# Kernel optimization log

Measured on AMD Instinct MI355X. Metric: run time of the kernel, lower is better.

Reference implementation:

```python
import jax, jax.numpy as jnp
import numpy as np

B, H, Wd, D, NC = 8, 64, 128, 272, 19   # batch, H/16, W/16, capsule feat dim, num_classes
P, NI = 524288, 4096                    # total points, total instances


def setup_inputs() -> dict:
    key = jax.random.key(0)
    k0, k1, k2, k3 = jax.random.split(key, 4)
    return {
        "class_capsules": jax.random.normal(k0, (B, H, Wd, D), dtype=jnp.float32),
        "W": jax.random.normal(k1, (D, NC), dtype=jnp.float32) * 0.05,
        "b": jnp.zeros((NC,), dtype=jnp.float32),
        "point_idx": jax.random.randint(k2, (P,), 0, B * H * Wd, dtype=jnp.int32),
        "segment_ids": jnp.sort(jax.random.randint(k3, (P,), 0, NI, dtype=jnp.int32)),
        "num_segments": NI,
    }


def reference(class_capsules, W, b, point_idx, segment_ids, num_segments):
    # Batched version of: inst_capsules = class_capsules[i, ys, xs, :];
    # pooled = mean(inst_capsules, 0); out = sigmoid(linear(pooled))
    # point_idx are flat (already deduped) indices into the [B*H*Wd] grid.
    feats = class_capsules.reshape(-1, class_capsules.shape[-1])[point_idx]        # [P, D]
    sums = jax.ops.segment_sum(feats, segment_ids, num_segments=num_segments)       # [NI, D]
    counts = jax.ops.segment_sum(jnp.ones((feats.shape[0],), feats.dtype),
                                 segment_ids, num_segments=num_segments)            # [NI]
    pooled = sums / jnp.maximum(counts, 1.0)[:, None]                                # mean pool
    return jax.nn.sigmoid(pooled @ W + b)                                            # [NI, NC]
```

## Files before the change

kernel.cpp:

```cpp
#include <hip/hip_runtime.h>
#include <math.h>

#define NROWS 65536
#define DD    272
#define NC    19
#define NP    524288
#define NSEG  4096
#define PS    20

#define PROJ_BLOCKS   (NROWS / 64)
#define BOUND_BLOCKS  (NP / 256)

__global__ __launch_bounds__(256) void proj_bounds_kernel(
    const float* __restrict__ X, const float* __restrict__ W,
    const int* __restrict__ seg, float* __restrict__ proj,
    int* __restrict__ bnd) {
  const int t = threadIdx.x;

  if (blockIdx.x >= PROJ_BLOCKS) {
    const int p = (blockIdx.x - PROJ_BLOCKS) * 256 + t;
    const int cur  = seg[p];
    const int prev = (p == 0) ? -1 : seg[p - 1];
    for (int s = prev + 1; s <= cur; ++s) bnd[s] = p;
    if (p == NP - 1) {
      for (int s = cur + 1; s <= NSEG; ++s) bnd[s] = NP;
    }
    return;
  }

  const int lane = t & 63;
  const int q    = __builtin_amdgcn_readfirstlane(t >> 6);
  const int row0 = blockIdx.x * 64;

  __shared__ float Xs[64 * 17];
  __shared__ float R[4 * 64 * NC];

  float acc[NC];
#pragma unroll
  for (int c = 0; c < NC; ++c) acc[c] = 0.f;

  const int r_ld = t >> 2;
  const int c4   = t & 3;
  const float* gsrc = X + (size_t)(row0 + r_ld) * DD + c4 * 4;

  float4 v = *(const float4*)gsrc;

  for (int chunk = 0; chunk < 17; ++chunk) {
    __syncthreads();
    float* dst = &Xs[r_ld * 17 + c4 * 4];
    dst[0] = v.x; dst[1] = v.y; dst[2] = v.z; dst[3] = v.w;
    __syncthreads();
    if (chunk < 16)
      v = *(const float4*)(gsrc + (chunk + 1) * 16);
    const int d0 = chunk * 16;
#pragma unroll
    for (int k = 0; k < 4; ++k) {
      const int c16 = q + 4 * k;
      const float x = Xs[lane * 17 + c16];
      const float* wr = W + (d0 + c16) * NC;
#pragma unroll
      for (int c = 0; c < NC; ++c) acc[c] = fmaf(x, wr[c], acc[c]);
    }
  }

#pragma unroll
  for (int c = 0; c < NC; ++c) R[(q * 64 + lane) * NC + c] = acc[c];
  __syncthreads();
#pragma unroll
  for (int j = 0; j < 5; ++j) {
    int f = t + 256 * j;
    int r = f / PS;
    int c = f % PS;
    float s = 0.f;
    if (c < NC) {
      s = R[r * NC + c] + R[(64 + r) * NC + c] +
          R[(128 + r) * NC + c] + R[(192 + r) * NC + c];
    }
    proj[(size_t)row0 * PS + f] = s;
  }
}

__global__ __launch_bounds__(64) void pool_kernel(
    const float* __restrict__ proj, const int* __restrict__ point_idx,
    const int* __restrict__ bnd, const float* __restrict__ bias,
    float* __restrict__ out) {
  const int s    = blockIdx.x;
  const int lane = threadIdx.x;
  const int start = bnd[s];
  const int end   = bnd[s + 1];

  float a[PS];
#pragma unroll
  for (int j = 0; j < PS; ++j) a[j] = 0.f;

  for (int p = start + lane; p < end; p += 64) {
    const int pi = point_idx[p];
    const float4* row = (const float4*)(proj + (size_t)pi * PS);
#pragma unroll
    for (int j = 0; j < 5; ++j) {
      float4 v = row[j];
      a[4 * j + 0] += v.x; a[4 * j + 1] += v.y;
      a[4 * j + 2] += v.z; a[4 * j + 3] += v.w;
    }
  }

#pragma unroll
  for (int off = 32; off > 0; off >>= 1) {
#pragma unroll
    for (int j = 0; j < NC; ++j) a[j] += __shfl_xor(a[j], off);
  }

  if (lane == 0) {
    const float inv = 1.f / fmaxf((float)(end - start), 1.f);
#pragma unroll
    for (int c = 0; c < NC; ++c) {
      float m = a[c] * inv + bias[c];
      out[s * NC + c] = 1.f / (1.f + expf(-m));
    }
  }
}

__global__ __launch_bounds__(256) void fallback_kernel(
    const float* __restrict__ X, const float* __restrict__ W,
    const float* __restrict__ bias, const int* __restrict__ point_idx,
    const int* __restrict__ seg, float* __restrict__ out) {
  const int s = blockIdx.x;
  const int t = threadIdx.x;
  __shared__ float Ps[DD];

  int lo = 0, hi = NP;
  while (lo < hi) { int mid = (lo + hi) >> 1; if (seg[mid] <  s) lo = mid + 1; else hi = mid; }
  const int start = lo;
  hi = NP;
  while (lo < hi) { int mid = (lo + hi) >> 1; if (seg[mid] <= s) lo = mid + 1; else hi = mid; }
  const int end = lo;

  float a0 = 0.f, a1 = 0.f;
  for (int p = start; p < end; ++p) {
    const int pi = point_idx[p];
    const float* row = X + (size_t)pi * DD;
    a0 += row[t];
    if (t < DD - 256) a1 += row[256 + t];
  }
  const float inv = 1.f / fmaxf((float)(end - start), 1.f);
  Ps[t] = a0 * inv;
  if (t < DD - 256) Ps[256 + t] = a1 * inv;
  __syncthreads();

  if (t < NC) {
    float acc = bias[t];
    for (int d = 0; d < DD; ++d) acc = fmaf(Ps[d], W[d * NC + t], acc);
    out[s * NC + t] = 1.f / (1.f + expf(-acc));
  }
}

extern "C" void kernel_launch(void* const* d_in, const int* in_sizes, int n_in,
                              void* d_out, int out_size, void* d_ws, size_t ws_size,
                              hipStream_t stream) {
  const float* X         = (const float*)d_in[0];
  const float* W         = (const float*)d_in[1];
  const float* bias      = (const float*)d_in[2];
  const int*   point_idx = (const int*)d_in[3];
  const int*   seg       = (const int*)d_in[4];
  float*       out       = (float*)d_out;

  const size_t proj_bytes = (size_t)NROWS * PS * sizeof(float);
  const size_t need = proj_bytes + (size_t)(NSEG + 1) * sizeof(int);
  if (ws_size >= need) {
    float* proj = (float*)d_ws;
    int*   bnd  = (int*)((char*)d_ws + proj_bytes);
    proj_bounds_kernel<<<PROJ_BLOCKS + BOUND_BLOCKS, 256, 0, stream>>>(
        X, W, seg, proj, bnd);
    pool_kernel<<<NSEG, 64, 0, stream>>>(proj, point_idx, bnd, bias, out);
  } else {
    fallback_kernel<<<NSEG, 256, 0, stream>>>(X, W, bias, point_idx, seg, out);
  }
}
```

Before: 128.7 us.

## Double-buffer projection tile loads and pack four segments per pool block

The projection kernel now double-buffers the shared-memory X tile and keeps two chunks of global loads in flight, which removes one barrier per chunk and hides load latency behind the FMAs. The pool kernel runs four segments per 256-thread block, one per wavefront, instead of one 64-thread block per segment. It also prefetches the next point index before the gathered row is accumulated. The trade-off is more shared memory and registers in the projection kernel.

```diff
diff --git a/kernel.cpp b/kernel.cpp
--- a/kernel.cpp
+++ b/kernel.cpp
@@ -32,7 +32,7 @@
   const int q    = __builtin_amdgcn_readfirstlane(t >> 6);
   const int row0 = blockIdx.x * 64;
 
-  __shared__ float Xs[64 * 17];
+  __shared__ float Xs[2][64 * 17];
   __shared__ float R[4 * 64 * NC];
 
   float acc[NC];
@@ -42,24 +42,37 @@
   const int r_ld = t >> 2;
   const int c4   = t & 3;
   const float* gsrc = X + (size_t)(row0 + r_ld) * DD + c4 * 4;
+  const int ldoff = r_ld * 17 + c4 * 4;
 
-  float4 v = *(const float4*)gsrc;
+  {
+    float4 v0 = *(const float4*)gsrc;
+    float* dst = &Xs[0][ldoff];
+    dst[0] = v0.x; dst[1] = v0.y; dst[2] = v0.z; dst[3] = v0.w;
+  }
+  float4 vv0 = *(const float4*)(gsrc + 16);
+  float4 vv1 = *(const float4*)(gsrc + 32);
+  __syncthreads();
 
   for (int chunk = 0; chunk < 17; ++chunk) {
-    __syncthreads();
-    float* dst = &Xs[r_ld * 17 + c4 * 4];
-    dst[0] = v.x; dst[1] = v.y; dst[2] = v.z; dst[3] = v.w;
-    __syncthreads();
-    if (chunk < 16)
-      v = *(const float4*)(gsrc + (chunk + 1) * 16);
     const int d0 = chunk * 16;
+    const float* xb = &Xs[chunk & 1][lane * 17];
 #pragma unroll
     for (int k = 0; k < 4; ++k) {
       const int c16 = q + 4 * k;
-      const float x = Xs[lane * 17 + c16];
+      const float x = xb[c16];
       const float* wr = W + (d0 + c16) * NC;
 #pragma unroll
       for (int c = 0; c < NC; ++c) acc[c] = fmaf(x, wr[c], acc[c]);
+    }
+    if (chunk < 16) {
+      float4 v = (chunk & 1) ? vv1 : vv0;
+      float* dst = &Xs[(chunk + 1) & 1][ldoff];
+      dst[0] = v.x; dst[1] = v.y; dst[2] = v.z; dst[3] = v.w;
+      __syncthreads();
+      if (chunk + 3 <= 16) {
+        float4 nv = *(const float4*)(gsrc + (chunk + 3) * 16);
+        if (chunk & 1) vv1 = nv; else vv0 = nv;
+      }
     }
   }
 
@@ -80,12 +93,13 @@
   }
 }
 
-__global__ __launch_bounds__(64) void pool_kernel(
+__global__ __launch_bounds__(256) void pool_kernel(
     const float* __restrict__ proj, const int* __restrict__ point_idx,
     const int* __restrict__ bnd, const float* __restrict__ bias,
     float* __restrict__ out) {
-  const int s    = blockIdx.x;
-  const int lane = threadIdx.x;
+  const int wave = threadIdx.x >> 6;
+  const int lane = threadIdx.x & 63;
+  const int s    = blockIdx.x * 4 + wave;
   const int start = bnd[s];
   const int end   = bnd[s + 1];
 
@@ -93,8 +107,11 @@
 #pragma unroll
   for (int j = 0; j < PS; ++j) a[j] = 0.f;
 
-  for (int p = start + lane; p < end; p += 64) {
-    const int pi = point_idx[p];
+  int p  = start + lane;
+  int pi = (p < end) ? point_idx[p] : 0;
+  while (p < end) {
+    const int pn  = p + 64;
+    const int pin = (pn < end) ? point_idx[pn] : 0;
     const float4* row = (const float4*)(proj + (size_t)pi * PS);
 #pragma unroll
     for (int j = 0; j < 5; ++j) {
@@ -102,6 +119,7 @@
       a[4 * j + 0] += v.x; a[4 * j + 1] += v.y;
       a[4 * j + 2] += v.z; a[4 * j + 3] += v.w;
     }
+    p = pn; pi = pin;
   }
 
 #pragma unroll
@@ -171,7 +189,7 @@
     int*   bnd  = (int*)((char*)d_ws + proj_bytes);
     proj_bounds_kernel<<<PROJ_BLOCKS + BOUND_BLOCKS, 256, 0, stream>>>(
         X, W, seg, proj, bnd);
-    pool_kernel<<<NSEG, 64, 0, stream>>>(proj, point_idx, bnd, bias, out);
+    pool_kernel<<<NSEG / 4, 256, 0, stream>>>(proj, point_idx, bnd, bias, out);
   } else {
     fallback_kernel<<<NSEG, 256, 0, stream>>>(X, W, bias, point_idx, seg, out);
   }
```

Result: no change. 130.4 us (+1.3%).
